# Kernel tuning notes

Hardware: AMD Instinct MI355X
Metric: run time of the kernel (lower is better)

The kernel has to match this reference:

```python
import jax, jax.numpy as jnp
import numpy as np


def setup_inputs() -> dict:
    key = jax.random.key(0)
    ks = jax.random.split(key, 12)
    B, N, M, C = 2, 20000, 4096, 6
    S, K, J = 2, 25, 64          # scales, grid cells (2*2+1)^2, neighbors per cell
    Cin = C + 2                   # xy coords concatenated to features
    Cout = 64
    xyz = jax.random.normal(ks[0], (B, N, 3), dtype=jnp.float32)
    feature = jax.random.normal(ks[1], (B, N, C), dtype=jnp.float32)
    new_xyz = jax.random.normal(ks[2], (B, M, 3), dtype=jnp.float32)
    idx = jax.random.randint(ks[3], (S, B, M, K, J), 0, N, dtype=jnp.int32)
    weight = jax.random.uniform(ks[4], (S, B, M, K, J), dtype=jnp.float32)
    conv_w = jax.random.normal(ks[5], (Cout, Cin, K), dtype=jnp.float32) * 0.05
    conv_b = jnp.zeros((Cout,), dtype=jnp.float32)
    mlp_w0 = jax.random.normal(ks[6], (128, S * Cout), dtype=jnp.float32) * 0.05
    mlp_b0 = jnp.zeros((128,), dtype=jnp.float32)
    mlp_w1 = jax.random.normal(ks[7], (256, 128), dtype=jnp.float32) * 0.05
    mlp_b1 = jnp.zeros((256,), dtype=jnp.float32)
    return {"xyz": xyz, "feature": feature, "new_xyz": new_xyz, "idx": idx,
            "weight": weight, "conv_w": conv_w, "conv_b": conv_b,
            "mlp_w0": mlp_w0, "mlp_b0": mlp_b0, "mlp_w1": mlp_w1, "mlp_b1": mlp_b1}


def reference(xyz, feature, new_xyz, idx, weight, conv_w, conv_b,
              mlp_w0, mlp_b0, mlp_w1, mlp_b1):
    # xyz_feature = cat(xy, feature): (B, N, Cin)
    xf = jnp.concatenate([xyz[:, :, :2], feature], axis=-1)
    center2 = new_xyz[:, :, :2]  # (B, M, 2); remaining channels of center are zero

    def per_scale(idx_s, w_s):
        # idx_s, w_s: (B, M, K, J). Gather neighbor features then bilinear-weight.
        gathered = jax.vmap(lambda f, i: f[i])(xf, idx_s)     # (B, M, K, J, Cin)
        nf = jnp.einsum('bmkj,bmkjc->bmkc', w_s, gathered)    # (B, M, K, Cin)
        nf = nf.at[..., :2].add(-center2[:, :, None, :])      # subtract center (xy only)
        # conv2d with kernel (1, K) over the neighbor axis + ReLU
        out = jnp.einsum('bmkc,ock->bom', nf, conv_w) + conv_b[None, :, None]
        return jax.nn.relu(out)                                # (B, Cout, M)

    outs = [per_scale(idx[s], weight[s]) for s in range(idx.shape[0])]
    x = jnp.concatenate(outs, axis=1)                          # (B, S*Cout, M)
    # SharedMLP: 1x1 convs with ReLU (bn=False)
    x = jax.nn.relu(jnp.einsum('bcm,oc->bom', x, mlp_w0) + mlp_b0[None, :, None])
    x = jax.nn.relu(jnp.einsum('bcm,oc->bom', x, mlp_w1) + mlp_b1[None, :, None])
    result_feature = jnp.transpose(x, (0, 2, 1))               # (B, M, 256)
    return new_xyz, result_feature
```

## Files before the change

### kernel.cpp

```cpp
#include <hip/hip_runtime.h>
#include <hip/hip_bf16.h>

#define B 2
#define N 20000
#define M 4096
#define S 2
#define K 25
#define J 64
#define KJ (K*J)
#define TC 32

__global__ __launch_bounds__(256) void prep_kernel(
    const float* __restrict__ xyz, const float* __restrict__ feature,
    const float* __restrict__ new_xyz, const float* __restrict__ conv_w,
    const float* __restrict__ w0, const float* __restrict__ w1,
    __hip_bfloat16* __restrict__ xfh, float* __restrict__ conv_wT,
    float* __restrict__ w0T, float* __restrict__ w1T,
    float* __restrict__ out_newxyz) {
    const int T1 = B * N * 8;
    const int T2 = 208 * 64;
    const int T3 = B * M * 3;
    const int T4 = 128 * 128;
    const int T5 = 128 * 256;
    int e = blockIdx.x * blockDim.x + threadIdx.x;
    if (e < T1) {
        int r = e >> 3, t = e & 7;
        float v = (t < 2) ? xyz[r * 3 + t] : feature[r * 6 + (t - 2)];
        xfh[e] = __float2bfloat16(v);
    } else if (e < T1 + T2) {
        int e2 = e - T1;
        int i = e2 >> 6, o = e2 & 63;
        conv_wT[e2] = (i < 200) ? conv_w[o * 200 + (i & 7) * 25 + (i >> 3)] : 0.f;
    } else if (e < T1 + T2 + T3) {
        int e3 = e - T1 - T2;
        out_newxyz[e3] = new_xyz[e3];
    } else if (e < T1 + T2 + T3 + T4) {
        int e4 = e - T1 - T2 - T3;
        int c = e4 >> 7, o = e4 & 127;
        w0T[e4] = w0[o * 128 + c];
    } else if (e < T1 + T2 + T3 + T4 + T5) {
        int e5 = e - T1 - T2 - T3 - T4;
        int c = e5 >> 8, o = e5 & 255;
        w1T[e5] = w1[o * 128 + c];
    }
}

__global__ __launch_bounds__(256) void gather_conv_kernel(
    const int* __restrict__ idx, const float* __restrict__ weight,
    const float* __restrict__ new_xyz, const uint4* __restrict__ xfh,
    const float* __restrict__ conv_wT, const float* __restrict__ conv_b,
    float* __restrict__ xmid) {
    __shared__ float snf[208];
    __shared__ float spart[4][64];

    int g = blockIdx.x;
    int m = g & (M - 1);
    int sb = g >> 12;
    int b = sb & (B - 1);
    int s = sb >> 1;
    int tid = threadIdx.x;

    if (tid >= 200 && tid < 208) snf[tid] = 0.f;

    if (tid < 200) {
        const int4*   gi4 = (const int4*)  (idx    + (size_t)g * KJ);
        const float4* gw4 = (const float4*)(weight + (size_t)g * KJ);
        int4   ia = gi4[tid * 2], ib = gi4[tid * 2 + 1];
        float4 wa = gw4[tid * 2], wb = gw4[tid * 2 + 1];

        const uint4* xfb = xfh + (size_t)b * N;
        float wsv[8]  = {wa.x, wa.y, wa.z, wa.w, wb.x, wb.y, wb.z, wb.w};

        uint4 r0, r1, r2, r3, r4, r5, r6, r7;
        {
            const uint4* a0 = xfb + ia.x;
            const uint4* a1 = xfb + ia.y;
            const uint4* a2 = xfb + ia.z;
            const uint4* a3 = xfb + ia.w;
            const uint4* a4 = xfb + ib.x;
            const uint4* a5 = xfb + ib.y;
            const uint4* a6 = xfb + ib.z;
            const uint4* a7 = xfb + ib.w;
            asm volatile(
                "global_load_dwordx4 %0, %8, off sc0\n\t"
                "global_load_dwordx4 %1, %9, off sc0\n\t"
                "global_load_dwordx4 %2, %10, off sc0\n\t"
                "global_load_dwordx4 %3, %11, off sc0\n\t"
                "global_load_dwordx4 %4, %12, off sc0\n\t"
                "global_load_dwordx4 %5, %13, off sc0\n\t"
                "global_load_dwordx4 %6, %14, off sc0\n\t"
                "global_load_dwordx4 %7, %15, off sc0\n\t"
                "s_waitcnt vmcnt(0)"
                : "=&v"(r0), "=&v"(r1), "=&v"(r2), "=&v"(r3),
                  "=&v"(r4), "=&v"(r5), "=&v"(r6), "=&v"(r7)
                : "v"(a0), "v"(a1), "v"(a2), "v"(a3),
                  "v"(a4), "v"(a5), "v"(a6), "v"(a7));
        }

        float acc[8] = {0.f,0.f,0.f,0.f,0.f,0.f,0.f,0.f};
        uint4 rr[8] = {r0, r1, r2, r3, r4, r5, r6, r7};
        #pragma unroll
        for (int j = 0; j < 8; ++j) {
            uint4 r = rr[j];
            float w = wsv[j];
            acc[0] = fmaf(w, __uint_as_float(r.x << 16),          acc[0]);
            acc[1] = fmaf(w, __uint_as_float(r.x & 0xffff0000u),  acc[1]);
            acc[2] = fmaf(w, __uint_as_float(r.y << 16),          acc[2]);
            acc[3] = fmaf(w, __uint_as_float(r.y & 0xffff0000u),  acc[3]);
            acc[4] = fmaf(w, __uint_as_float(r.z << 16),          acc[4]);
            acc[5] = fmaf(w, __uint_as_float(r.z & 0xffff0000u),  acc[5]);
            acc[6] = fmaf(w, __uint_as_float(r.w << 16),          acc[6]);
            acc[7] = fmaf(w, __uint_as_float(r.w & 0xffff0000u),  acc[7]);
        }
        #pragma unroll
        for (int d = 1; d < 8; d <<= 1) {
            #pragma unroll
            for (int c = 0; c < 8; ++c) acc[c] += __shfl_xor(acc[c], d, 64);
        }
        if ((tid & 7) == 0) {
            int kk = tid >> 3;
            float cx = new_xyz[(b * M + m) * 3 + 0];
            float cy = new_xyz[(b * M + m) * 3 + 1];
            acc[0] -= cx; acc[1] -= cy;
            float4* s4 = (float4*)&snf[kk * 8];
            s4[0] = make_float4(acc[0], acc[1], acc[2], acc[3]);
            s4[1] = make_float4(acc[4], acc[5], acc[6], acc[7]);
        }
    }
    __syncthreads();

    int o = tid & 63, p = tid >> 6;
    const float4* snf4 = (const float4*)snf;
    float acc2 = 0.f;
    #pragma unroll
    for (int q = 0; q < 13; ++q) {
        float4 v = snf4[p * 13 + q];
        int i = (p * 13 + q) * 4;
        acc2 = fmaf(v.x, conv_wT[(i + 0) * 64 + o], acc2);
        acc2 = fmaf(v.y, conv_wT[(i + 1) * 64 + o], acc2);
        acc2 = fmaf(v.z, conv_wT[(i + 2) * 64 + o], acc2);
        acc2 = fmaf(v.w, conv_wT[(i + 3) * 64 + o], acc2);
    }
    spart[p][o] = acc2;
    __syncthreads();

    if (tid < 64) {
        float v = spart[0][tid] + spart[1][tid] + spart[2][tid] + spart[3][tid] + conv_b[tid];
        v = fmaxf(v, 0.f);
        xmid[((size_t)(b * M + m)) * 128 + s * 64 + tid] = v;
    }
}

__global__ __launch_bounds__(256) void mlp0_kernel(
    float* __restrict__ xmid,
    const float* __restrict__ w0T, const float* __restrict__ b0) {
    __shared__ float ws[128 * 128];
    __shared__ float xs[128 * 32];

    int tid = threadIdx.x;
    int col0 = blockIdx.x * TC;

    {
        const float4* w4 = (const float4*)w0T;
        float4* ws4 = (float4*)ws;
        #pragma unroll
        for (int i = 0; i < 16; ++i) ws4[tid + 256 * i] = w4[tid + 256 * i];
    }
    {
        const float4* xm4 = (const float4*)(xmid + (size_t)col0 * 128);
        #pragma unroll
        for (int r = tid; r < 1024; r += 256) {
            int lc = r >> 5, c4 = r & 31;
            float4 v = xm4[lc * 32 + c4];
            int c = c4 * 4;
            xs[(c + 0) * 32 + lc] = v.x;
            xs[(c + 1) * 32 + lc] = v.y;
            xs[(c + 2) * 32 + lc] = v.z;
            xs[(c + 3) * 32 + lc] = v.w;
        }
    }
    __syncthreads();

    int og = tid >> 3, cg = tid & 7;
    int o0 = og * 4, lc0 = cg * 4;
    float acc[4][4];
    #pragma unroll
    for (int i = 0; i < 4; ++i) {
        float bv = b0[o0 + i];
        #pragma unroll
        for (int u = 0; u < 4; ++u) acc[i][u] = bv;
    }
    for (int c = 0; c < 128; ++c) {
        float4 xv = *(const float4*)&xs[c * 32 + lc0];
        float4 wv = *(const float4*)&ws[c * 128 + o0];
        acc[0][0] = fmaf(wv.x, xv.x, acc[0][0]);
        acc[0][1] = fmaf(wv.x, xv.y, acc[0][1]);
        acc[0][2] = fmaf(wv.x, xv.z, acc[0][2]);
        acc[0][3] = fmaf(wv.x, xv.w, acc[0][3]);
        acc[1][0] = fmaf(wv.y, xv.x, acc[1][0]);
        acc[1][1] = fmaf(wv.y, xv.y, acc[1][1]);
        acc[1][2] = fmaf(wv.y, xv.z, acc[1][2]);
        acc[1][3] = fmaf(wv.y, xv.w, acc[1][3]);
        acc[2][0] = fmaf(wv.z, xv.x, acc[2][0]);
        acc[2][1] = fmaf(wv.z, xv.y, acc[2][1]);
        acc[2][2] = fmaf(wv.z, xv.z, acc[2][2]);
        acc[2][3] = fmaf(wv.z, xv.w, acc[2][3]);
        acc[3][0] = fmaf(wv.w, xv.x, acc[3][0]);
        acc[3][1] = fmaf(wv.w, xv.y, acc[3][1]);
        acc[3][2] = fmaf(wv.w, xv.z, acc[3][2]);
        acc[3][3] = fmaf(wv.w, xv.w, acc[3][3]);
    }
    #pragma unroll
    for (int u = 0; u < 4; ++u) {
        float4 v = make_float4(fmaxf(acc[0][u], 0.f), fmaxf(acc[1][u], 0.f),
                               fmaxf(acc[2][u], 0.f), fmaxf(acc[3][u], 0.f));
        *(float4*)&xmid[(size_t)(col0 + lc0 + u) * 128 + o0] = v;
    }
}

__global__ __launch_bounds__(256) void mlp1_kernel(
    const float* __restrict__ xmid,
    const float* __restrict__ w1T, const float* __restrict__ b1,
    float* __restrict__ out_rf) {
    __shared__ float ws[128 * 128];
    __shared__ float xs[128 * 32];

    int tid = threadIdx.x;
    int bx = blockIdx.x;
    int col0 = (bx >> 1) * TC;
    int oH = (bx & 1) * 128;

    {
        for (int i = tid; i < 4096; i += 256) {
            int c = i >> 5, q = i & 31;
            *(float4*)&ws[c * 128 + q * 4] = *(const float4*)&w1T[c * 256 + oH + q * 4];
        }
    }
    {
        const float4* xm4 = (const float4*)(xmid + (size_t)col0 * 128);
        #pragma unroll
        for (int r = tid; r < 1024; r += 256) {
            int lc = r >> 5, c4 = r & 31;
            float4 v = xm4[lc * 32 + c4];
            int c = c4 * 4;
            xs[(c + 0) * 32 + lc] = v.x;
            xs[(c + 1) * 32 + lc] = v.y;
            xs[(c + 2) * 32 + lc] = v.z;
            xs[(c + 3) * 32 + lc] = v.w;
        }
    }
    __syncthreads();

    int og = tid >> 3, cg = tid & 7;
    int o0 = og * 4, lc0 = cg * 4;
    float acc[4][4];
    #pragma unroll
    for (int i = 0; i < 4; ++i) {
        float bv = b1[oH + o0 + i];
        #pragma unroll
        for (int u = 0; u < 4; ++u) acc[i][u] = bv;
    }
    for (int c = 0; c < 128; ++c) {
        float4 xv = *(const float4*)&xs[c * 32 + lc0];
        float4 wv = *(const float4*)&ws[c * 128 + o0];
        acc[0][0] = fmaf(wv.x, xv.x, acc[0][0]);
        acc[0][1] = fmaf(wv.x, xv.y, acc[0][1]);
        acc[0][2] = fmaf(wv.x, xv.z, acc[0][2]);
        acc[0][3] = fmaf(wv.x, xv.w, acc[0][3]);
        acc[1][0] = fmaf(wv.y, xv.x, acc[1][0]);
        acc[1][1] = fmaf(wv.y, xv.y, acc[1][1]);
        acc[1][2] = fmaf(wv.y, xv.z, acc[1][2]);
        acc[1][3] = fmaf(wv.y, xv.w, acc[1][3]);
        acc[2][0] = fmaf(wv.z, xv.x, acc[2][0]);
        acc[2][1] = fmaf(wv.z, xv.y, acc[2][1]);
        acc[2][2] = fmaf(wv.z, xv.z, acc[2][2]);
        acc[2][3] = fmaf(wv.z, xv.w, acc[2][3]);
        acc[3][0] = fmaf(wv.w, xv.x, acc[3][0]);
        acc[3][1] = fmaf(wv.w, xv.y, acc[3][1]);
        acc[3][2] = fmaf(wv.w, xv.z, acc[3][2]);
        acc[3][3] = fmaf(wv.w, xv.w, acc[3][3]);
    }
    #pragma unroll
    for (int u = 0; u < 4; ++u) {
        float4 v = make_float4(fmaxf(acc[0][u], 0.f), fmaxf(acc[1][u], 0.f),
                               fmaxf(acc[2][u], 0.f), fmaxf(acc[3][u], 0.f));
        *(float4*)&out_rf[(size_t)(col0 + lc0 + u) * 256 + oH + o0] = v;
    }
}

extern "C" void kernel_launch(void* const* d_in, const int* in_sizes, int n_in,
                              void* d_out, int out_size, void* d_ws, size_t ws_size,
                              hipStream_t stream) {
    const float* xyz     = (const float*)d_in[0];
    const float* feature = (const float*)d_in[1];
    const float* new_xyz = (const float*)d_in[2];
    const int*   idx     = (const int*)  d_in[3];
    const float* weight  = (const float*)d_in[4];
    const float* conv_w  = (const float*)d_in[5];
    const float* conv_b  = (const float*)d_in[6];
    const float* mlp_w0  = (const float*)d_in[7];
    const float* mlp_b0  = (const float*)d_in[8];
    const float* mlp_w1  = (const float*)d_in[9];
    const float* mlp_b1  = (const float*)d_in[10];

    float* out    = (float*)d_out;
    float* out_rf = out + (size_t)B * M * 3;

    float* wsf = (float*)d_ws;
    __hip_bfloat16* xfh = (__hip_bfloat16*)wsf;
    float* conv_wT = wsf + 160000;
    float* xmid    = conv_wT + 13312;
    float* w0T     = xmid + 1048576;
    float* w1T     = w0T + 16384;

    {
        int total = 320000 + 13312 + 24576 + 16384 + 32768;
        int blocks = (total + 255) / 256;
        prep_kernel<<<blocks, 256, 0, stream>>>(xyz, feature, new_xyz, conv_w,
                                                mlp_w0, mlp_w1,
                                                xfh, conv_wT, w0T, w1T, out);
    }
    {
        int blocks = S * B * M;
        gather_conv_kernel<<<blocks, 256, 0, stream>>>(idx, weight, new_xyz,
                                                       (const uint4*)xfh,
                                                       conv_wT, conv_b, xmid);
    }
    {
        mlp0_kernel<<<(B * M) / TC, 256, 0, stream>>>(xmid, w0T, mlp_b0);
    }
    {
        mlp1_kernel<<<2 * (B * M) / TC, 256, 0, stream>>>(xmid, w1T, mlp_b1, out_rf);
    }
}
```

Measured before the change: 363.3 us.

## Stage half of the feature table in LDS and use wave-per-group gather-conv

The gather-conv kernel now uses 1024-thread blocks that each handle 64 (scale, batch, center) groups. Each block first copies the first 10176 bf16 feature rows of its batch into shared memory, about 160KB. Gathers with indices below that bound read from LDS and the rest go to global memory. The conv reduction is restructured so each wave does one group via shuffles, with no shared staging or extra syncs. The per-block preload of 160KB is redundant across 128 blocks, and the large LDS footprint limits occupancy to one block per CU.

```diff
diff --git a/kernel.cpp b/kernel.cpp
--- a/kernel.cpp
+++ b/kernel.cpp
@@ -9,6 +9,10 @@
 #define J 64
 #define KJ (K*J)
 #define TC 32
+
+#define CHUNK 10176
+#define GPB   64
+#define NTH   1024
 
 __global__ __launch_bounds__(256) void prep_kernel(
     const float* __restrict__ xyz, const float* __restrict__ feature,
@@ -45,109 +49,89 @@
     }
 }
 
-__global__ __launch_bounds__(256) void gather_conv_kernel(
+__global__ __launch_bounds__(NTH) void gather_conv_kernel(
     const int* __restrict__ idx, const float* __restrict__ weight,
     const float* __restrict__ new_xyz, const uint4* __restrict__ xfh,
     const float* __restrict__ conv_wT, const float* __restrict__ conv_b,
     float* __restrict__ xmid) {
-    __shared__ float snf[208];
-    __shared__ float spart[4][64];
-
-    int g = blockIdx.x;
-    int m = g & (M - 1);
-    int sb = g >> 12;
-    int b = sb & (B - 1);
-    int s = sb >> 1;
-    int tid = threadIdx.x;
-
-    if (tid >= 200 && tid < 208) snf[tid] = 0.f;
-
-    if (tid < 200) {
-        const int4*   gi4 = (const int4*)  (idx    + (size_t)g * KJ);
-        const float4* gw4 = (const float4*)(weight + (size_t)g * KJ);
-        int4   ia = gi4[tid * 2], ib = gi4[tid * 2 + 1];
-        float4 wa = gw4[tid * 2], wb = gw4[tid * 2 + 1];
-
-        const uint4* xfb = xfh + (size_t)b * N;
-        float wsv[8]  = {wa.x, wa.y, wa.z, wa.w, wb.x, wb.y, wb.z, wb.w};
-
-        uint4 r0, r1, r2, r3, r4, r5, r6, r7;
-        {
-            const uint4* a0 = xfb + ia.x;
-            const uint4* a1 = xfb + ia.y;
-            const uint4* a2 = xfb + ia.z;
-            const uint4* a3 = xfb + ia.w;
-            const uint4* a4 = xfb + ib.x;
-            const uint4* a5 = xfb + ib.y;
-            const uint4* a6 = xfb + ib.z;
-            const uint4* a7 = xfb + ib.w;
-            asm volatile(
-                "global_load_dwordx4 %0, %8, off sc0\n\t"
-                "global_load_dwordx4 %1, %9, off sc0\n\t"
-                "global_load_dwordx4 %2, %10, off sc0\n\t"
-                "global_load_dwordx4 %3, %11, off sc0\n\t"
-                "global_load_dwordx4 %4, %12, off sc0\n\t"
-                "global_load_dwordx4 %5, %13, off sc0\n\t"
-                "global_load_dwordx4 %6, %14, off sc0\n\t"
-                "global_load_dwordx4 %7, %15, off sc0\n\t"
-                "s_waitcnt vmcnt(0)"
-                : "=&v"(r0), "=&v"(r1), "=&v"(r2), "=&v"(r3),
-                  "=&v"(r4), "=&v"(r5), "=&v"(r6), "=&v"(r7)
-                : "v"(a0), "v"(a1), "v"(a2), "v"(a3),
-                  "v"(a4), "v"(a5), "v"(a6), "v"(a7));
+    __shared__ uint4 chunk[CHUNK];
+
+    const int tid = threadIdx.x;
+    const int g0  = blockIdx.x * GPB;
+    const int b   = (g0 >> 12) & (B - 1);
+    const uint4* xfb = xfh + (size_t)b * N;
+
+    for (int r = tid; r < CHUNK; r += NTH) chunk[r] = xfb[r];
+    __syncthreads();
+
+    const int team = tid >> 6;
+    const int lane = tid & 63;
+    const float bo = conv_b[lane];
+
+    for (int u = 0; u < GPB / (NTH / 64); ++u) {
+        const int g = g0 + team * (GPB / (NTH / 64)) + u;
+        const int m = g & (M - 1);
+        const int s = g >> 13;
+        const float cx = new_xyz[(b * M + m) * 3 + 0];
+        const float cy = new_xyz[(b * M + m) * 3 + 1];
+        float acc2 = bo;
+
+        #pragma unroll 1
+        for (int p = 0; p < 4; ++p) {
+            const int myk = p * 8 + (lane >> 3);
+            const bool act = (p < 3) || (lane < 8);
+            float acc[8] = {0.f,0.f,0.f,0.f,0.f,0.f,0.f,0.f};
+            if (act) {
+                const size_t base = (size_t)g * KJ + (size_t)myk * J + (lane & 7) * 8;
+                const int4   ia = *(const int4*)  (idx + base);
+                const int4   ib = *(const int4*)  (idx + base + 4);
+                const float4 wa = *(const float4*)(weight + base);
+                const float4 wb = *(const float4*)(weight + base + 4);
+                const int   ids[8] = {ia.x, ia.y, ia.z, ia.w, ib.x, ib.y, ib.z, ib.w};
+                const float wsv[8] = {wa.x, wa.y, wa.z, wa.w, wb.x, wb.y, wb.z, wb.w};
+
+                uint4 rr[8];
+                #pragma unroll
+                for (int j = 0; j < 8; ++j)
+                    if (ids[j] < CHUNK) rr[j] = chunk[ids[j]];
+                #pragma unroll
+                for (int j = 0; j < 8; ++j)
+                    if (ids[j] >= CHUNK) rr[j] = xfb[ids[j]];
+
+                #pragma unroll
+                for (int j = 0; j < 8; ++j) {
+                    const uint4 r = rr[j];
+                    const float w = wsv[j];
+                    acc[0] = fmaf(w, __uint_as_float(r.x << 16),         acc[0]);
+                    acc[1] = fmaf(w, __uint_as_float(r.x & 0xffff0000u), acc[1]);
+                    acc[2] = fmaf(w, __uint_as_float(r.y << 16),         acc[2]);
+                    acc[3] = fmaf(w, __uint_as_float(r.y & 0xffff0000u), acc[3]);
+                    acc[4] = fmaf(w, __uint_as_float(r.z << 16),         acc[4]);
+                    acc[5] = fmaf(w, __uint_as_float(r.z & 0xffff0000u), acc[5]);
+                    acc[6] = fmaf(w, __uint_as_float(r.w << 16),         acc[6]);
+                    acc[7] = fmaf(w, __uint_as_float(r.w & 0xffff0000u), acc[7]);
+                }
+                #pragma unroll
+                for (int d = 1; d < 8; d <<= 1) {
+                    #pragma unroll
+                    for (int c = 0; c < 8; ++c) acc[c] += __shfl_xor(acc[c], d, 64);
+                }
+                if ((lane & 7) == 0) { acc[0] -= cx; acc[1] -= cy; }
+            }
+            const int nk = (p < 3) ? 8 : 1;
+            #pragma unroll
+            for (int kk = 0; kk < 8; ++kk) {
+                if (kk < nk) {
+                    const float* wrow = conv_wT + (size_t)((p * 8 + kk) * 8) * 64 + lane;
+                    #pragma unroll
+                    for (int c = 0; c < 8; ++c) {
+                        const float v = __shfl(acc[c], kk * 8, 64);
+                        acc2 = fmaf(v, wrow[c * 64], acc2);
+                    }
+                }
+            }
         }
-
-        float acc[8] = {0.f,0.f,0.f,0.f,0.f,0.f,0.f,0.f};
-        uint4 rr[8] = {r0, r1, r2, r3, r4, r5, r6, r7};
-        #pragma unroll
-        for (int j = 0; j < 8; ++j) {
-            uint4 r = rr[j];
-            float w = wsv[j];
-            acc[0] = fmaf(w, __uint_as_float(r.x << 16),          acc[0]);
-            acc[1] = fmaf(w, __uint_as_float(r.x & 0xffff0000u),  acc[1]);
-            acc[2] = fmaf(w, __uint_as_float(r.y << 16),          acc[2]);
-            acc[3] = fmaf(w, __uint_as_float(r.y & 0xffff0000u),  acc[3]);
-            acc[4] = fmaf(w, __uint_as_float(r.z << 16),          acc[4]);
-            acc[5] = fmaf(w, __uint_as_float(r.z & 0xffff0000u),  acc[5]);
-            acc[6] = fmaf(w, __uint_as_float(r.w << 16),          acc[6]);
-            acc[7] = fmaf(w, __uint_as_float(r.w & 0xffff0000u),  acc[7]);
-        }
-        #pragma unroll
-        for (int d = 1; d < 8; d <<= 1) {
-            #pragma unroll
-            for (int c = 0; c < 8; ++c) acc[c] += __shfl_xor(acc[c], d, 64);
-        }
-        if ((tid & 7) == 0) {
-            int kk = tid >> 3;
-            float cx = new_xyz[(b * M + m) * 3 + 0];
-            float cy = new_xyz[(b * M + m) * 3 + 1];
-            acc[0] -= cx; acc[1] -= cy;
-            float4* s4 = (float4*)&snf[kk * 8];
-            s4[0] = make_float4(acc[0], acc[1], acc[2], acc[3]);
-            s4[1] = make_float4(acc[4], acc[5], acc[6], acc[7]);
-        }
-    }
-    __syncthreads();
-
-    int o = tid & 63, p = tid >> 6;
-    const float4* snf4 = (const float4*)snf;
-    float acc2 = 0.f;
-    #pragma unroll
-    for (int q = 0; q < 13; ++q) {
-        float4 v = snf4[p * 13 + q];
-        int i = (p * 13 + q) * 4;
-        acc2 = fmaf(v.x, conv_wT[(i + 0) * 64 + o], acc2);
-        acc2 = fmaf(v.y, conv_wT[(i + 1) * 64 + o], acc2);
-        acc2 = fmaf(v.z, conv_wT[(i + 2) * 64 + o], acc2);
-        acc2 = fmaf(v.w, conv_wT[(i + 3) * 64 + o], acc2);
-    }
-    spart[p][o] = acc2;
-    __syncthreads();
-
-    if (tid < 64) {
-        float v = spart[0][tid] + spart[1][tid] + spart[2][tid] + spart[3][tid] + conv_b[tid];
-        v = fmaxf(v, 0.f);
-        xmid[((size_t)(b * M + m)) * 128 + s * 64 + tid] = v;
+        xmid[((size_t)(b * M + m)) * 128 + s * 64 + lane] = fmaxf(acc2, 0.f);
     }
 }
 
@@ -321,8 +305,8 @@
                                                 xfh, conv_wT, w0T, w1T, out);
     }
     {
-        int blocks = S * B * M;
-        gather_conv_kernel<<<blocks, 256, 0, stream>>>(idx, weight, new_xyz,
+        int blocks = (S * B * M) / GPB;
+        gather_conv_kernel<<<blocks, NTH, 0, stream>>>(idx, weight, new_xyz,
                                                        (const uint4*)xfh,
                                                        conv_wT, conv_b, xmid);
     }
```

Result: faster. 347.3 us (-4.4%).
